# Performance work log

Hardware: AMD Instinct MI355X
Metric: run time of the kernel (lower is better)

The kernel has to match this reference:

```python
import jax, jax.numpy as jnp
import numpy as np

N_NODES = 25000
N_EDGES = 400000
FEAT = 128
N_CH = 32
FEAT_OUT = 128
N_OUT = 32
P = 6
NUM_NEIGHBORS = 16.0
INV_SQRT3 = 1.0 / np.sqrt(3.0)


def _envelope_coeffs(n0, n1):
    # unique poly of degree n0+n1+1 with f(0)=1, derivs 1..n0 zero at 0,
    # f(1)=0 and derivs 1..n1 zero at 1  (== e3nn.poly_envelope(n0, n1))
    D = n0 + n1 + 1
    powers = np.arange(n0 + 1, D + 1)
    m = n1 + 1
    A = np.zeros((m, m)); b = np.zeros(m)
    for k in range(m):
        for ji, j in enumerate(powers):
            A[k, ji] = np.prod(np.arange(j, j - k, -1.0))  # falling factorial j!/(j-k)!
        b[k] = -1.0 if k == 0 else 0.0
    return powers, np.linalg.solve(A, b)

_POW, _COEF = _envelope_coeffs(P - 1, 2)


def envelope(d):
    poly = 1.0 + sum(float(c) * d ** int(j) for j, c in zip(_POW, _COEF))
    return jnp.where(d < 1.0, poly, 0.0)


def safe_norm(x, axis=None):
    x2 = jnp.sum(x ** 2, axis=axis)
    return jnp.where(x2 == 0, 1, x2) ** 0.5


def setup_inputs():
    key = jax.random.key(0)
    ks = jax.random.split(key, 10)
    x = jax.random.normal(ks[0], (N_EDGES, FEAT), jnp.float32)
    V = jax.random.normal(ks[1], (N_EDGES, N_CH, 4), jnp.float32)
    r = 0.3 * jax.random.normal(ks[2], (N_EDGES, 3), jnp.float32)  # norms mostly < cutoff 1
    Y = jax.random.normal(ks[3], (N_EDGES, 4), jnp.float32)        # irreps 0e+1o
    edge_src = jax.random.randint(ks[4], (N_EDGES,), 0, N_NODES)
    W1 = jax.random.normal(ks[5], (FEAT, N_CH), jnp.float32)
    W2a = jax.random.normal(ks[6], (FEAT + 2 * N_CH, FEAT_OUT), jnp.float32)
    W2b = jax.random.normal(ks[7], (FEAT_OUT, FEAT_OUT), jnp.float32)
    W2c = jax.random.normal(ks[8], (FEAT_OUT, FEAT_OUT), jnp.float32)
    Wlin = jax.random.normal(ks[9], (2 * N_CH, N_OUT), jnp.float32)
    return dict(x=x, V=V, r=r, Y=Y, edge_src=edge_src,
                W1=W1, W2a=W2a, W2b=W2b, W2c=W2c, Wlin=Wlin)


def reference(x, V, r, Y, edge_src, W1, W2a, W2b, W2c, Wlin):
    E, F = x.shape
    n = V.shape[1]
    d = safe_norm(r, axis=1)                               # (E,)
    # edge MLP (e3nn MLP with one layer, no activation; 1/sqrt(fan_in) weight norm)
    w = (x @ W1) / jnp.sqrt(F)                             # (E, n)
    wY = w[:, :, None] * Y[:, None, :]                     # (E, n, 4) irreps 0e+1o
    # index_add over edge_src with map_back=True
    agg = jax.ops.segment_sum(wY, edge_src, num_segments=N_NODES)
    wY = agg[edge_src] / jnp.sqrt(NUM_NEIGHBORS)           # (E, n, 4)
    # CG tensor product wY (x) V, filter_ir_out = 0e + 1o  (component normalization)
    a_s, a_v = wY[..., 0], wY[..., 1:4]
    b_s, b_v = V[..., 0], V[..., 1:4]
    s1 = a_s * b_s                                         # 0e x 0e -> 0e
    s2 = jnp.sum(a_v * b_v, axis=-1) * INV_SQRT3           # 1o x 1o -> 0e
    v1 = a_s[..., None] * b_v                              # 0e x 1o -> 1o
    v2 = a_v * b_s[..., None]                              # 1o x 0e -> 1o
    # scalars: filter(keep='0e').axis_to_mul() -> (E, 2n), concat with x
    scalars = jnp.stack([s1, s2], axis=-1).reshape(E, 2 * n)
    h = jnp.concatenate([x, scalars], axis=1)              # (E, F + 2n)
    # 3-layer silu MLP, no output activation, 1/sqrt(fan_in) weight norm
    h = jax.nn.silu((h @ W2a) / jnp.sqrt(F + 2 * n))
    h = jax.nn.silu((h @ W2b) / jnp.sqrt(FEAT_OUT))
    h = (h @ W2c) / jnp.sqrt(FEAT_OUT)
    x_out = envelope(d)[:, None] * h                       # (E, FEAT_OUT)
    # V: axis_to_mul -> (E, 2n x 1o); equivariant Linear -> n_out x 1o; mul_to_axis
    Vv = jnp.stack([v1, v2], axis=2).reshape(E, 2 * n, 3)
    V_out = jnp.einsum('eui,uv->evi', Vv, Wlin) / jnp.sqrt(2 * n)  # (E, n_out, 3)
    return x_out, V_out
```

## Files before the change

kernel.cpp:

```cpp
#include <hip/hip_runtime.h>

#define NE 400000
#define NNODES 25000

typedef __attribute__((ext_vector_type(8))) short short8;
typedef __attribute__((ext_vector_type(4))) float f32x4;

#define W2A_H 0
#define W2A_L 24576
#define W2B_H 49152
#define W2B_L 65536
#define W2C_H 81920
#define W2C_L 98304
#define WLIN_H 114688
#define WLIN_L 116736
#define W1_H   118784
#define W1_L   122880

__device__ __forceinline__ unsigned short f2bf(float f) {
  unsigned int u = __float_as_uint(f);
  unsigned int r = u + 0x7fffu + ((u >> 16) & 1u);
  return (unsigned short)(r >> 16);
}
__device__ __forceinline__ float bf2f(unsigned short h) {
  return __uint_as_float(((unsigned int)h) << 16);
}
__device__ __forceinline__ unsigned int cvtpk(float lo, float hi) {
  unsigned int r;
  asm("v_cvt_pk_bf16_f32 %0, %1, %2" : "=v"(r) : "v"(lo), "v"(hi));
  return r;
}
__device__ __forceinline__ float fsilu(float z) {
  return z * __builtin_amdgcn_rcpf(1.f + __expf(-z));
}

__global__ __launch_bounds__(256) void khist(const int* __restrict__ esrc,
                                             int* __restrict__ cnt) {
  int e = blockIdx.x * 256 + threadIdx.x;
  if (e < NE) atomicAdd(&cnt[esrc[e]], 1);
}

__global__ __launch_bounds__(1024) void kscan(const int* __restrict__ cnt,
                                              int* __restrict__ start,
                                              int* __restrict__ cursor) {
  __shared__ int wsum[16];
  __shared__ int carry_s;
  const int t = threadIdx.x;
  const int lane = t & 63, wid = t >> 6;
  if (t == 0) carry_s = 0;
  __syncthreads();
  for (int base = 0; base < NNODES; base += 1024) {
    int idx = base + t;
    int v = (idx < NNODES) ? cnt[idx] : 0;
    int incl = v;
    #pragma unroll
    for (int off = 1; off < 64; off <<= 1) {
      int u = __shfl_up(incl, off, 64);
      if (lane >= off) incl += u;
    }
    if (lane == 63) wsum[wid] = incl;
    __syncthreads();
    if (wid == 0) {
      int wv = (lane < 16) ? wsum[lane] : 0;
      int wincl = wv;
      #pragma unroll
      for (int off = 1; off < 16; off <<= 1) {
        int u = __shfl_up(wincl, off, 64);
        if (lane >= off) wincl += u;
      }
      if (lane < 16) wsum[lane] = wincl - wv;
    }
    __syncthreads();
    int excl = incl - v + wsum[wid] + carry_s;
    if (idx < NNODES) { start[idx] = excl; cursor[idx] = excl; }
    __syncthreads();
    if (t == 1023) carry_s = excl + v;
    __syncthreads();
  }
  if (t == 0) start[NNODES] = carry_s;
}

__global__ __launch_bounds__(256) void kfill(const int* __restrict__ esrc,
                                             int* __restrict__ cursor,
                                             int* __restrict__ order) {
  int e = blockIdx.x * 256 + threadIdx.x;
  if (e < NE) {
    int p = atomicAdd(&cursor[esrc[e]], 1);
    order[p] = e;
  }
}

__global__ __launch_bounds__(256) void kprep(
    const float* __restrict__ W2a, const float* __restrict__ W2b,
    const float* __restrict__ W2c, const float* __restrict__ Wlin,
    const float* __restrict__ W1, unsigned short* __restrict__ wp)
{
  int tid = blockIdx.x * 256 + threadIdx.x;
  if (tid < 7168) {
    int gi = tid;
    const float* W; float sc; unsigned short* outh; int K;
    if (gi < 3072)      { W = W2a; sc = 0.07216878364870323f; outh = wp + W2A_H; K = 192; }
    else if (gi < 5120) { W = W2b; sc = 0.08838834764831845f; outh = wp + W2B_H; K = 128; gi -= 3072; }
    else                { W = W2c; sc = 0.08838834764831845f; outh = wp + W2C_H; K = 128; gi -= 5120; }
    unsigned short* outl = outh + K * 128;
    int l15 = gi & 15, l4 = (gi >> 4) & 3, c16 = (gi >> 6) & 7, kc5 = gi >> 9;
    #pragma unroll
    for (int j = 0; j < 8; ++j) {
      int k = kc5 * 32 + l4 * 8 + j;
      int n = c16 * 16 + l15;
      float v = W[(size_t)k * 128 + n] * sc;
      unsigned short h = f2bf(v);
      outh[gi * 8 + j] = h;
      outl[gi * 8 + j] = f2bf(v - bf2f(h));
    }
  } else if (tid < 7424) {
    int gi = tid - 7168;
    int l15 = gi & 15, l4 = (gi >> 4) & 3, nt = (gi >> 6) & 1, kc2 = gi >> 7;
    #pragma unroll
    for (int j = 0; j < 8; ++j) {
      int k = kc2 * 32 + l4 * 8 + j;
      int n = nt * 16 + l15;
      float v = Wlin[(size_t)k * 32 + n] * 0.125f;
      unsigned short h = f2bf(v);
      wp[WLIN_H + gi * 8 + j] = h;
      wp[WLIN_L + gi * 8 + j] = f2bf(v - bf2f(h));
    }
  } else if (tid < 7936) {
    int gi = tid - 7424;
    int l15 = gi & 15, l4 = (gi >> 4) & 3, nf = (gi >> 6) & 1, kc5 = gi >> 7;
    #pragma unroll
    for (int j = 0; j < 8; ++j) {
      int k = kc5 * 32 + l4 * 8 + j;
      int n = nf * 16 + l15;
      float v = W1[(size_t)k * 32 + n] * 0.08838834764831845f;
      unsigned short h = f2bf(v);
      wp[W1_H + gi * 8 + j] = h;
      wp[W1_L + gi * 8 + j] = f2bf(v - bf2f(h));
    }
  }
}

__global__ __launch_bounds__(256) void k1w(
    const float* __restrict__ x, const unsigned short* __restrict__ wp,
    float* __restrict__ wbuf, unsigned short* __restrict__ xh)
{
  const int t = threadIdx.x;
  const int w = t >> 6, lane = t & 63;
  const int l15 = lane & 15, l4 = lane >> 4;
  const int e0 = blockIdx.x * 128;

  f32x4 acc[2][2];
  #pragma unroll
  for (int i = 0; i < 2; ++i)
    #pragma unroll
    for (int j = 0; j < 2; ++j) acc[i][j] = (f32x4)(0.f);

  #pragma unroll
  for (int kc5 = 0; kc5 < 4; ++kc5) {
    short8 bh[2], bl[2];
    #pragma unroll
    for (int nf = 0; nf < 2; ++nf) {
      int idx = (((kc5 * 2 + nf) * 4 + l4) * 16 + l15) * 8;
      bh[nf] = *(const short8*)&wp[W1_H + idx];
      bl[nf] = *(const short8*)&wp[W1_L + idx];
    }
    #pragma unroll
    for (int mf = 0; mf < 2; ++mf) {
      const int row = w * 32 + mf * 16 + l15;
      const float* xp = x + (size_t)(e0 + row) * 128 + kc5 * 32 + l4 * 8;
      float a8[8];
      *(float4*)&a8[0] = *(const float4*)xp;
      *(float4*)&a8[4] = *(const float4*)(xp + 4);
      short8 ah, al;
      #pragma unroll
      for (int j = 0; j < 8; ++j) {
        unsigned short h = f2bf(a8[j]);
        ah[j] = (short)h;
        al[j] = (short)f2bf(a8[j] - bf2f(h));
      }
      *(uint4*)&xh[(size_t)blockIdx.x * 16384 + kc5 * 4096 +
                   (w * 2 + mf) * 512 + l4 * 128 + l15 * 8] = *(uint4*)&ah;
      #pragma unroll
      for (int nf = 0; nf < 2; ++nf) {
        acc[mf][nf] = __builtin_amdgcn_mfma_f32_16x16x32_bf16(ah, bh[nf], acc[mf][nf], 0, 0, 0);
        acc[mf][nf] = __builtin_amdgcn_mfma_f32_16x16x32_bf16(ah, bl[nf], acc[mf][nf], 0, 0, 0);
        acc[mf][nf] = __builtin_amdgcn_mfma_f32_16x16x32_bf16(al, bh[nf], acc[mf][nf], 0, 0, 0);
      }
    }
  }
  #pragma unroll
  for (int mf = 0; mf < 2; ++mf)
    #pragma unroll
    for (int nf = 0; nf < 2; ++nf)
      #pragma unroll
      for (int rr = 0; rr < 4; ++rr) {
        int row = e0 + w * 32 + mf * 16 + l4 * 4 + rr;
        wbuf[(size_t)row * 32 + nf * 16 + l15] = acc[mf][nf][rr];
      }
}

__global__ __launch_bounds__(64) void k_agg(
    const float* __restrict__ wbuf, const float* __restrict__ Y,
    const int* __restrict__ start, const int* __restrict__ order,
    float* __restrict__ agg)
{
  const int n = blockIdx.x;
  const int t = threadIdx.x;
  const int c = t & 31;
  const int dh = t >> 5;
  const int s0 = start[n], s1 = start[n + 1];
  float a0 = 0.f, a1 = 0.f;
  for (int i = s0; i < s1; ++i) {
    int e = order[i];
    float wv = wbuf[(size_t)e * 32 + c];
    float y0 = Y[e * 4 + dh * 2 + 0];
    float y1 = Y[e * 4 + dh * 2 + 1];
    a0 += wv * y0;
    a1 += wv * y1;
  }
  float* ap = agg + (size_t)n * 128 + c * 4 + dh * 2;
  ap[0] = a0;
  ap[1] = a1;
}

__global__ __launch_bounds__(256, 4) void kfused(
    const unsigned short* __restrict__ xh, const float* __restrict__ V,
    const float* __restrict__ r, const int* __restrict__ esrc,
    const float* __restrict__ agg, const unsigned short* __restrict__ wp,
    float* __restrict__ xout, float* __restrict__ vout)
{
  __shared__ __align__(16) char lds[32768];

  const int t = threadIdx.x;
  const int w = t >> 6, lane = t & 63;
  const int wr = w >> 1, wc = w & 1;
  const int l15 = lane & 15, l4 = lane >> 4;
  const int e0 = blockIdx.x * 64;

  {
    const int er = w * 16 + l15;
    const int e = e0 + er;
    const int src = esrc[e];
    f32x4 accv[3][2];
    #pragma unroll
    for (int i = 0; i < 3; ++i)
      #pragma unroll
      for (int nt = 0; nt < 2; ++nt) accv[i][nt] = (f32x4)(0.f);

    #pragma unroll
    for (int kc2 = 0; kc2 < 2; ++kc2) {
      short8 WhF[2], WlF[2];
      #pragma unroll
      for (int nt = 0; nt < 2; ++nt) {
        int idx = ((((kc2 * 2 + nt) * 4 + l4) * 16) + l15) * 8;
        WhF[nt] = *(const short8*)&wp[WLIN_H + idx];
        WlF[nt] = *(const short8*)&wp[WLIN_L + idx];
      }
      float4 av4[4], bv4[4];
      const float* ap = agg + (size_t)src * 128 + kc2 * 64 + l4 * 16;
      const float* bp = V + (size_t)e * 128 + kc2 * 64 + l4 * 16;
      #pragma unroll
      for (int j = 0; j < 4; ++j) {
        av4[j] = *(const float4*)(ap + j * 4);
        bv4[j] = *(const float4*)(bp + j * 4);
        av4[j].x *= 0.25f; av4[j].y *= 0.25f; av4[j].z *= 0.25f; av4[j].w *= 0.25f;
      }
      unsigned int su[4];
      #pragma unroll
      for (int ch = 0; ch < 4; ++ch) {
        float s1 = av4[ch].x * bv4[ch].x;
        float s2 = (av4[ch].y * bv4[ch].y + av4[ch].z * bv4[ch].z +
                    av4[ch].w * bv4[ch].w) * 0.5773502691896258f;
        su[ch] = cvtpk(s1, s2);
      }
      {
        int byte = er * 256 + (kc2 * 32 + l4 * 8) * 2;
        byte ^= (er & 7) << 4;
        *(uint4*)(lds + byte) = *(uint4*)su;
      }
      #pragma unroll
      for (int i = 0; i < 3; ++i) {
        union { unsigned int u[4]; short8 s; } ahu;
        #pragma unroll
        for (int ch = 0; ch < 4; ++ch) {
          float bvi = (i == 0) ? bv4[ch].y : (i == 1) ? bv4[ch].z : bv4[ch].w;
          float avi = (i == 0) ? av4[ch].y : (i == 1) ? av4[ch].z : av4[ch].w;
          ahu.u[ch] = cvtpk(av4[ch].x * bvi, avi * bv4[ch].x);
        }
        #pragma unroll
        for (int nt = 0; nt < 2; ++nt) {
          accv[i][nt] = __builtin_amdgcn_mfma_f32_16x16x32_bf16(ahu.s, WhF[nt], accv[i][nt], 0, 0, 0);
          accv[i][nt] = __builtin_amdgcn_mfma_f32_16x16x32_bf16(ahu.s, WlF[nt], accv[i][nt], 0, 0, 0);
        }
      }
    }
    const int ebase = e0 + w * 16 + l4 * 4;
    #pragma unroll
    for (int nt = 0; nt < 2; ++nt)
      #pragma unroll
      for (int rr = 0; rr < 4; ++rr) {
        float* vp = vout + (size_t)(ebase + rr) * 96 + (nt * 16 + l15) * 3;
        vp[0] = accv[0][nt][rr];
        vp[1] = accv[1][nt][rr];
        vp[2] = accv[2][nt][rr];
      }
  }

  __syncthreads();

  f32x4 acc[2][4];
  const int c16 = wc * 4;
  const size_t T16 = (size_t)(blockIdx.x >> 1) * 16384;
  const int xb1 = blockIdx.x & 1;

  #pragma unroll
  for (int i = 0; i < 2; ++i)
    #pragma unroll
    for (int j = 0; j < 4; ++j) acc[i][j] = (f32x4)(0.f);

  #pragma unroll
  for (int kc5 = 0; kc5 < 6; ++kc5) {
    short8 bh[4];
    #pragma unroll
    for (int nf = 0; nf < 4; ++nf) {
      int idx = (((kc5 * 8 + c16 + nf) * 4 + l4) * 16 + l15) * 8;
      bh[nf] = *(const short8*)&wp[W2A_H + idx];
    }
    #pragma unroll
    for (int mf = 0; mf < 2; ++mf) {
      short8 ah;
      if (kc5 < 4) {
        ah = *(const short8*)&xh[T16 + kc5 * 4096 + xb1 * 2048 +
                                 (wr * 2 + mf) * 512 + l4 * 128 + l15 * 8];
      } else {
        int ar = wr * 32 + mf * 16 + l15;
        int byte = ar * 256 + ((kc5 - 4) * 32 + l4 * 8) * 2;
        byte ^= (ar & 7) << 4;
        ah = *(const short8*)(lds + byte);
      }
      #pragma unroll
      for (int nf = 0; nf < 4; ++nf)
        acc[mf][nf] = __builtin_amdgcn_mfma_f32_16x16x32_bf16(ah, bh[nf], acc[mf][nf], 0, 0, 0);
    }
  }

  #pragma unroll
  for (int mf = 0; mf < 2; ++mf)
    #pragma unroll
    for (int nf = 0; nf < 4; ++nf)
      #pragma unroll
      for (int rp = 0; rp < 2; ++rp) {
        unsigned int zz = cvtpk(fsilu(acc[mf][nf][2 * rp]), fsilu(acc[mf][nf][2 * rp + 1]));
        #pragma unroll
        for (int rh = 0; rh < 2; ++rh) {
          int row = wr * 32 + mf * 16 + l4 * 4 + 2 * rp + rh;
          int byte = row * 256 + (wc * 64 + nf * 16 + l15) * 2;
          byte ^= (row & 7) << 4;
          *(unsigned short*)(lds + 16384 + byte) = (unsigned short)(zz >> (16 * rh));
        }
      }

  __syncthreads();

  #pragma unroll
  for (int i = 0; i < 2; ++i)
    #pragma unroll
    for (int j = 0; j < 4; ++j) acc[i][j] = (f32x4)(0.f);

  #pragma unroll
  for (int kc5 = 0; kc5 < 4; ++kc5) {
    short8 bh[4];
    #pragma unroll
    for (int nf = 0; nf < 4; ++nf) {
      int idx = (((kc5 * 8 + c16 + nf) * 4 + l4) * 16 + l15) * 8;
      bh[nf] = *(const short8*)&wp[W2B_H + idx];
    }
    #pragma unroll
    for (int mf = 0; mf < 2; ++mf) {
      int row = wr * 32 + mf * 16 + l15;
      int byte = row * 256 + (kc5 * 32 + l4 * 8) * 2;
      byte ^= (row & 7) << 4;
      short8 ah = *(const short8*)(lds + 16384 + byte);
      #pragma unroll
      for (int nf = 0; nf < 4; ++nf)
        acc[mf][nf] = __builtin_amdgcn_mfma_f32_16x16x32_bf16(ah, bh[nf], acc[mf][nf], 0, 0, 0);
    }
  }

  #pragma unroll
  for (int mf = 0; mf < 2; ++mf)
    #pragma unroll
    for (int nf = 0; nf < 4; ++nf)
      #pragma unroll
      for (int rp = 0; rp < 2; ++rp) {
        unsigned int zz = cvtpk(fsilu(acc[mf][nf][2 * rp]), fsilu(acc[mf][nf][2 * rp + 1]));
        #pragma unroll
        for (int rh = 0; rh < 2; ++rh) {
          int row = wr * 32 + mf * 16 + l4 * 4 + 2 * rp + rh;
          int byte = row * 256 + (wc * 64 + nf * 16 + l15) * 2;
          byte ^= (row & 7) << 4;
          *(unsigned short*)(lds + byte) = (unsigned short)(zz >> (16 * rh));
        }
      }

  __syncthreads();

  #pragma unroll
  for (int i = 0; i < 2; ++i)
    #pragma unroll
    for (int j = 0; j < 4; ++j) acc[i][j] = (f32x4)(0.f);

  #pragma unroll
  for (int kc5 = 0; kc5 < 4; ++kc5) {
    short8 bh[4];
    #pragma unroll
    for (int nf = 0; nf < 4; ++nf) {
      int idx = (((kc5 * 8 + c16 + nf) * 4 + l4) * 16 + l15) * 8;
      bh[nf] = *(const short8*)&wp[W2C_H + idx];
    }
    #pragma unroll
    for (int mf = 0; mf < 2; ++mf) {
      int row = wr * 32 + mf * 16 + l15;
      int byte = row * 256 + (kc5 * 32 + l4 * 8) * 2;
      byte ^= (row & 7) << 4;
      short8 ah = *(const short8*)(lds + byte);
      #pragma unroll
      for (int nf = 0; nf < 4; ++nf)
        acc[mf][nf] = __builtin_amdgcn_mfma_f32_16x16x32_bf16(ah, bh[nf], acc[mf][nf], 0, 0, 0);
    }
  }

  #pragma unroll
  for (int mf = 0; mf < 2; ++mf) {
    float env4[4];
    #pragma unroll
    for (int rr = 0; rr < 4; ++rr) {
      int row = e0 + wr * 32 + mf * 16 + l4 * 4 + rr;
      float rx = r[row * 3 + 0];
      float ry = r[row * 3 + 1];
      float rz = r[row * 3 + 2];
      float d2 = rx * rx + ry * ry + rz * rz;
      float d = (d2 == 0.f) ? 1.f : sqrtf(d2);
      float d3 = d * d * d;
      env4[rr] = (d < 1.f) ? (1.f + d3 * d3 * (-28.f + d * (48.f - 21.f * d))) : 0.f;
    }
    #pragma unroll
    for (int nf = 0; nf < 4; ++nf)
      #pragma unroll
      for (int rr = 0; rr < 4; ++rr) {
        int row = e0 + wr * 32 + mf * 16 + l4 * 4 + rr;
        xout[(size_t)row * 128 + wc * 64 + nf * 16 + l15] = acc[mf][nf][rr] * env4[rr];
      }
  }
}

extern "C" void kernel_launch(void* const* d_in, const int* in_sizes, int n_in,
                              void* d_out, int out_size, void* d_ws, size_t ws_size,
                              hipStream_t stream)
{
  const float* x    = (const float*)d_in[0];
  const float* V    = (const float*)d_in[1];
  const float* r    = (const float*)d_in[2];
  const float* Y    = (const float*)d_in[3];
  const int*   es   = (const int*)d_in[4];
  const float* W1   = (const float*)d_in[5];
  const float* W2a  = (const float*)d_in[6];
  const float* W2b  = (const float*)d_in[7];
  const float* W2c  = (const float*)d_in[8];
  const float* Wlin = (const float*)d_in[9];

  float* ws   = (float*)d_ws;
  float* agg  = ws;
  float* wbuf = ws + 3200000;
  unsigned short* xh = (unsigned short*)(ws + 16000000);
  int*   ci   = (int*)(ws + 42000000);
  int*   cnt    = ci;
  int*   startv = ci + 25000;
  int*   cursor = ci + 50008;
  int*   order  = ci + 75008;
  unsigned short* wp = (unsigned short*)(ws + 43000000);
  float* xout = (float*)d_out;
  float* vout = (float*)d_out + 51200000;

  (void)in_sizes; (void)n_in; (void)out_size; (void)ws_size;

  hipMemsetAsync(cnt, 0, NNODES * sizeof(int), stream);
  khist<<<dim3((NE + 255) / 256), 256, 0, stream>>>(es, cnt);
  kscan<<<dim3(1), 1024, 0, stream>>>(cnt, startv, cursor);
  kfill<<<dim3((NE + 255) / 256), 256, 0, stream>>>(es, cursor, order);
  kprep<<<dim3(31), 256, 0, stream>>>(W2a, W2b, W2c, Wlin, W1, wp);
  k1w<<<dim3(NE / 128), 256, 0, stream>>>(x, wp, wbuf, xh);
  k_agg<<<dim3(NNODES), 64, 0, stream>>>(wbuf, Y, startv, order, agg);
  kfused<<<dim3(NE / 64), 256, 0, stream>>>(xh, V, r, es, agg, wp, xout, vout);
}
```

Before: 413.7 us.

## Fuse histogram into k1w, parallelize node scan, prefetch x fragments in kfused

The separate histogram kernel is removed and its atomic counting moves into the k1w GEMM kernel. The single-block serial prefix scan becomes a three-kernel multi-block scan (block scan, scan of block sums, add-back). kfused also loads its x bf16 fragments into registers at kernel start, so those loads overlap with the V/Wlin stage. The aim is fewer launches, less serial scan latency, and hidden global load latency, at the cost of extra registers in kfused and more kernel launches for the scan.

New measurement: 375.1 us. -9.3%, faster.

```diff
diff --git a/kernel.cpp b/kernel.cpp
--- a/kernel.cpp
+++ b/kernel.cpp
@@ -34,50 +34,61 @@
   return z * __builtin_amdgcn_rcpf(1.f + __expf(-z));
 }
 
-__global__ __launch_bounds__(256) void khist(const int* __restrict__ esrc,
-                                             int* __restrict__ cnt) {
-  int e = blockIdx.x * 256 + threadIdx.x;
-  if (e < NE) atomicAdd(&cnt[esrc[e]], 1);
-}
-
-__global__ __launch_bounds__(1024) void kscan(const int* __restrict__ cnt,
+__global__ __launch_bounds__(256) void kscanA(const int* __restrict__ cnt,
+                                              int* __restrict__ start,
+                                              int* __restrict__ sums) {
+  __shared__ int wtot[4];
+  const int t = threadIdx.x, lane = t & 63, wid = t >> 6;
+  const int idx = blockIdx.x * 256 + t;
+  int v = (idx < NNODES) ? cnt[idx] : 0;
+  int incl = v;
+  #pragma unroll
+  for (int off = 1; off < 64; off <<= 1) {
+    int u = __shfl_up(incl, off, 64);
+    if (lane >= off) incl += u;
+  }
+  if (lane == 63) wtot[wid] = incl;
+  __syncthreads();
+  int woff = 0;
+  #pragma unroll
+  for (int i = 0; i < 4; ++i)
+    if (i < wid) woff += wtot[i];
+  int excl = incl - v + woff;
+  if (idx < NNODES) start[idx] = excl;
+  if (t == 255) sums[blockIdx.x] = excl + v;
+}
+
+__global__ __launch_bounds__(64) void kscanB(int* __restrict__ sums) {
+  const int lane = threadIdx.x & 63;
+  int a = (lane < 98) ? sums[lane] : 0;
+  int b = (64 + lane < 98) ? sums[64 + lane] : 0;
+  int ia = a;
+  #pragma unroll
+  for (int off = 1; off < 64; off <<= 1) {
+    int u = __shfl_up(ia, off, 64);
+    if (lane >= off) ia += u;
+  }
+  int total_a = __shfl(ia, 63, 64);
+  int ib = b;
+  #pragma unroll
+  for (int off = 1; off < 64; off <<= 1) {
+    int u = __shfl_up(ib, off, 64);
+    if (lane >= off) ib += u;
+  }
+  if (lane < 98) sums[lane] = ia - a;
+  if (64 + lane < 98) sums[64 + lane] = total_a + ib - b;
+}
+
+__global__ __launch_bounds__(256) void kscanC(const int* __restrict__ sums,
                                               int* __restrict__ start,
                                               int* __restrict__ cursor) {
-  __shared__ int wsum[16];
-  __shared__ int carry_s;
-  const int t = threadIdx.x;
-  const int lane = t & 63, wid = t >> 6;
-  if (t == 0) carry_s = 0;
-  __syncthreads();
-  for (int base = 0; base < NNODES; base += 1024) {
-    int idx = base + t;
-    int v = (idx < NNODES) ? cnt[idx] : 0;
-    int incl = v;
-    #pragma unroll
-    for (int off = 1; off < 64; off <<= 1) {
-      int u = __shfl_up(incl, off, 64);
-      if (lane >= off) incl += u;
-    }
-    if (lane == 63) wsum[wid] = incl;
-    __syncthreads();
-    if (wid == 0) {
-      int wv = (lane < 16) ? wsum[lane] : 0;
-      int wincl = wv;
-      #pragma unroll
-      for (int off = 1; off < 16; off <<= 1) {
-        int u = __shfl_up(wincl, off, 64);
-        if (lane >= off) wincl += u;
-      }
-      if (lane < 16) wsum[lane] = wincl - wv;
-    }
-    __syncthreads();
-    int excl = incl - v + wsum[wid] + carry_s;
-    if (idx < NNODES) { start[idx] = excl; cursor[idx] = excl; }
-    __syncthreads();
-    if (t == 1023) carry_s = excl + v;
-    __syncthreads();
-  }
-  if (t == 0) start[NNODES] = carry_s;
+  const int idx = blockIdx.x * 256 + threadIdx.x;
+  if (idx < NNODES) {
+    int s = start[idx] + sums[blockIdx.x];
+    start[idx] = s;
+    cursor[idx] = s;
+  }
+  if (idx == 0) start[NNODES] = NE;
 }
 
 __global__ __launch_bounds__(256) void kfill(const int* __restrict__ esrc,
@@ -142,12 +153,15 @@
 
 __global__ __launch_bounds__(256) void k1w(
     const float* __restrict__ x, const unsigned short* __restrict__ wp,
+    const int* __restrict__ esrc, int* __restrict__ cnt,
     float* __restrict__ wbuf, unsigned short* __restrict__ xh)
 {
   const int t = threadIdx.x;
   const int w = t >> 6, lane = t & 63;
   const int l15 = lane & 15, l4 = lane >> 4;
   const int e0 = blockIdx.x * 128;
+
+  if (t < 128) atomicAdd(&cnt[esrc[e0 + t]], 1);
 
   f32x4 acc[2][2];
   #pragma unroll
@@ -236,6 +250,16 @@
   const int wr = w >> 1, wc = w & 1;
   const int l15 = lane & 15, l4 = lane >> 4;
   const int e0 = blockIdx.x * 64;
+  const size_t T16 = (size_t)(blockIdx.x >> 1) * 16384;
+  const int xb1 = blockIdx.x & 1;
+
+  short8 xfrag[4][2];
+  #pragma unroll
+  for (int kc5 = 0; kc5 < 4; ++kc5)
+    #pragma unroll
+    for (int mf = 0; mf < 2; ++mf)
+      xfrag[kc5][mf] = *(const short8*)&xh[T16 + kc5 * 4096 + xb1 * 2048 +
+                                           (wr * 2 + mf) * 512 + l4 * 128 + l15 * 8];
 
   {
     const int er = w * 16 + l15;
@@ -310,8 +334,6 @@
 
   f32x4 acc[2][4];
   const int c16 = wc * 4;
-  const size_t T16 = (size_t)(blockIdx.x >> 1) * 16384;
-  const int xb1 = blockIdx.x & 1;
 
   #pragma unroll
   for (int i = 0; i < 2; ++i)
@@ -330,8 +352,7 @@
     for (int mf = 0; mf < 2; ++mf) {
       short8 ah;
       if (kc5 < 4) {
-        ah = *(const short8*)&xh[T16 + kc5 * 4096 + xb1 * 2048 +
-                                 (wr * 2 + mf) * 512 + l4 * 128 + l15 * 8];
+        ah = xfrag[kc5][mf];
       } else {
         int ar = wr * 32 + mf * 16 + l15;
         int byte = ar * 256 + ((kc5 - 4) * 32 + l4 * 8) * 2;
@@ -478,6 +499,7 @@
   int*   startv = ci + 25000;
   int*   cursor = ci + 50008;
   int*   order  = ci + 75008;
+  int*   sums   = ci + 480000;
   unsigned short* wp = (unsigned short*)(ws + 43000000);
   float* xout = (float*)d_out;
   float* vout = (float*)d_out + 51200000;
@@ -485,11 +507,12 @@
   (void)in_sizes; (void)n_in; (void)out_size; (void)ws_size;
 
   hipMemsetAsync(cnt, 0, NNODES * sizeof(int), stream);
-  khist<<<dim3((NE + 255) / 256), 256, 0, stream>>>(es, cnt);
-  kscan<<<dim3(1), 1024, 0, stream>>>(cnt, startv, cursor);
+  kprep<<<dim3(31), 256, 0, stream>>>(W2a, W2b, W2c, Wlin, W1, wp);
+  k1w<<<dim3(NE / 128), 256, 0, stream>>>(x, wp, es, cnt, wbuf, xh);
+  kscanA<<<dim3(98), 256, 0, stream>>>(cnt, startv, sums);
+  kscanB<<<dim3(1), 64, 0, stream>>>(sums);
+  kscanC<<<dim3(98), 256, 0, stream>>>(sums, startv, cursor);
   kfill<<<dim3((NE + 255) / 256), 256, 0, stream>>>(es, cursor, order);
-  kprep<<<dim3(31), 256, 0, stream>>>(W2a, W2b, W2c, Wlin, W1, wp);
-  k1w<<<dim3(NE / 128), 256, 0, stream>>>(x, wp, wbuf, xh);
   k_agg<<<dim3(NNODES), 64, 0, stream>>>(wbuf, Y, startv, order, agg);
   kfused<<<dim3(NE / 64), 256, 0, stream>>>(xh, V, r, es, agg, wp, xout, vout);
 }
```
